# Optimization experiments

Hardware: AMD Instinct MI355X
Metric: run time of the kernel (lower is better)

## Reference

```python
import jax, jax.numpy as jnp
import numpy as np

M, N, DV, DC, ITERS = 512, 1024, 3, 6, 10
BATCH = 8192
ATANH_CLIP = 0.999995


def _build_graph():
    """Deterministic (3,6)-regular Tanner graph, edge order = row-major nonzeros of H."""
    offsets = [0, 1, 2, 512, 515, 519]
    H = np.zeros((M, N), np.int64)
    r = np.arange(M)
    for off in offsets:
        H[r, (2 * r + off) % N] = 1
    ei, ej = np.nonzero(H)                       # E = M*DC = 3072 edges, row-major
    E = ei.size
    var2edges = np.argsort(ej, kind='stable').reshape(N, DV)   # edges of each variable
    chk2edges = np.argsort(ei, kind='stable').reshape(M, DC)   # edges of each check
    v_sum = np.empty((E, DV - 1), np.int64)      # for edge e: other edges on same variable
    c_prod = np.empty((E, DC - 1), np.int64)     # for edge e: other edges on same check
    for e in range(E):
        gv = var2edges[ej[e]]
        v_sum[e] = gv[gv != e]
        gc = chk2edges[ei[e]]
        c_prod[e] = gc[gc != e]
    return v_sum, c_prod, ej.astype(np.int64), var2edges


def setup_inputs() -> dict:
    key = jax.random.key(0)
    ks = jax.random.split(key, 6)
    v_sum, c_prod, edge_var, var2edges = _build_graph()
    E = edge_var.shape[0]                        # 3072
    TW = E * (DV - 1)                            # total_weights = 6144
    return {
        "llr": jax.random.normal(ks[0], (BATCH, N), jnp.float32),
        "w_iter": 1.0 + 0.1 * jax.random.normal(ks[1], (ITERS, TW), jnp.float32),
        "llr_iter": 1.0 + 0.1 * jax.random.normal(ks[2], (ITERS, N), jnp.float32),
        "w_final": 1.0 + 0.1 * jax.random.normal(ks[3], (E,), jnp.float32),
        "llr_final": 1.0 + 0.1 * jax.random.normal(ks[4], (N,), jnp.float32),
        "v_sum_idx": jnp.asarray(v_sum),         # [E, DV-1]
        "c_prod_idx": jnp.asarray(c_prod),       # [E, DC-1]
        "edge_var": jnp.asarray(edge_var),       # [E] variable index of each edge
        "final_idx": jnp.asarray(var2edges),     # [N, DV] edges feeding each variable marginal
    }


def reference(llr, w_iter, llr_iter, w_final, llr_final,
              v_sum_idx, c_prod_idx, edge_var, final_idx):
    B = llr.shape[0]
    E = edge_var.shape[0]
    c2v0 = jnp.zeros((B, E), llr.dtype)

    def bp_iter(c2v, params):
        w, lw = params                                      # [E*(DV-1)], [N]
        # variable -> check: weighted sum of extrinsic c2v messages + weighted LLR
        s = (c2v[:, v_sum_idx] * w.reshape(E, DV - 1)).sum(-1)        # [B,E]
        v2c = jnp.tanh(0.5 * (s + (llr * lw)[:, edge_var]))           # [B,E]
        # check -> variable: product of extrinsic v2c messages, 2*atanh
        prods = v2c[:, c_prod_idx].prod(-1)                           # [B,E]
        return 2.0 * jnp.arctanh(ATANH_CLIP * prods), None

    c2v, _ = jax.lax.scan(bp_iter, c2v0, (w_iter, llr_iter))
    # final marginalization: per-variable sum of weighted incoming messages
    fin = (c2v[:, final_idx.reshape(-1)] * w_final).reshape(B, N, DV).sum(-1)
    out = fin + llr * llr_final
    return jax.nn.sigmoid(out[:, : N - M])
```

## Files before the change

### kernel.cpp

```cpp
#include <hip/hip_runtime.h>
#include <hip/hip_bf16.h>


namespace {

constexpr int T      = 512;
constexpr int ROWS   = 2;
constexpr int MCHK   = 512;
constexpr int NVAR   = 1024;
constexpr int EEDG   = 3072;
constexpr int NITER  = 10;
constexpr int STRIDE = 7;
constexpr int BATCH  = 8192;
constexpr int NOUT   = 512;

constexpr float LOG2E = 1.4426950408889634f;
constexpr float LN2   = 0.6931471805599453f;
constexpr float KAPPA = 0.999995f;

__device__ __forceinline__ float fast_exp2(float x) { return __builtin_amdgcn_exp2f(x); }
__device__ __forceinline__ float fast_log2(float x) { return __builtin_amdgcn_logf(x); }
__device__ __forceinline__ float fast_rcp (float x) { return __builtin_amdgcn_rcpf(x); }

__global__ __launch_bounds__(T, 4)
void bp_decode(const float* __restrict__ llr,
               const float* __restrict__ w_iter,
               const float* __restrict__ llr_iter,
               const float* __restrict__ w_final,
               const float* __restrict__ llr_final,
               const int*  __restrict__ v_sum_idx,
               const int*  __restrict__ edge_var,
               const int*  __restrict__ final_idx,
               float* __restrict__ out)
{
    __shared__ float2 Ad[MCHK * STRIDE];

    const int  tid = threadIdx.x;
    const long b0  = (long)blockIdx.x * ROWS;

    #pragma unroll
    for (int k = 0; k < STRIDE; ++k)
        Ad[k * T + tid] = make_float2(0.f, 0.f);

    int nb[12];
    {
        const int4* p = (const int4*)(v_sum_idx + 12 * tid);
        int4 q0 = p[0], q1 = p[1], q2 = p[2];
        nb[0]=q0.x; nb[1]=q0.y; nb[2]=q0.z; nb[3]=q0.w;
        nb[4]=q1.x; nb[5]=q1.y; nb[6]=q1.z; nb[7]=q1.w;
        nb[8]=q2.x; nb[9]=q2.y; nb[10]=q2.z; nb[11]=q2.w;
    }
    int goff[12];
    #pragma unroll
    for (int j = 0; j < 12; ++j)
        goff[j] = (nb[j] / 6) * STRIDE + (nb[j] % 6);

    int var[6];
    {
        const int2* p = (const int2*)(edge_var + 6 * tid);
        int2 q0 = p[0], q1 = p[1], q2 = p[2];
        var[0]=q0.x; var[1]=q0.y; var[2]=q1.x; var[3]=q1.y; var[4]=q2.x; var[5]=q2.y;
    }

    float Lx[6], Ly[6];
    #pragma unroll
    for (int j = 0; j < 6; ++j) {
        Lx[j] = llr[ b0      * NVAR + var[j]];
        Ly[j] = llr[(b0 + 1) * NVAR + var[j]];
    }

    __syncthreads();

    const int own = STRIDE * tid;

    #pragma unroll 1
    for (int it = 0; it < NITER; ++it) {
        const float* wit = w_iter + it * (EEDG * 2) + 12 * tid;
        float4 wa = ((const float4*)wit)[0];
        float4 wb = ((const float4*)wit)[1];
        float4 wc = ((const float4*)wit)[2];
        float w[12] = {wa.x,wa.y,wa.z,wa.w, wb.x,wb.y,wb.z,wb.w, wc.x,wc.y,wc.z,wc.w};

        const float* lit = llr_iter + it * NVAR;
        float li[6];
        #pragma unroll
        for (int j = 0; j < 6; ++j) li[j] = lit[var[j]] * LOG2E;

        float2 g[12];
        #pragma unroll
        for (int j = 0; j < 12; ++j) g[j] = Ad[goff[j]];

        __syncthreads();

        float tx[6], ty[6];
        #pragma unroll
        for (int j = 0; j < 6; ++j) {
            float ax = fmaf(w[2*j], g[2*j].x, fmaf(w[2*j+1], g[2*j+1].x, Lx[j]*li[j]));
            float ay = fmaf(w[2*j], g[2*j].y, fmaf(w[2*j+1], g[2*j+1].y, Ly[j]*li[j]));
            float zx = fast_exp2(ax);
            float zy = fast_exp2(ay);
            tx[j] = fmaf(-2.f, fast_rcp(zx + 1.f), 1.f);
            ty[j] = fmaf(-2.f, fast_rcp(zy + 1.f), 1.f);
        }

        float px[6], py[6];
        {
            float P1=tx[0], P2=P1*tx[1], P3=P2*tx[2], P4=P3*tx[3], P5=P4*tx[4];
            float S4=tx[5], S3=S4*tx[4], S2=S3*tx[3], S1=S2*tx[2], S0=S1*tx[1];
            px[0]=S0; px[1]=P1*S1; px[2]=P2*S2; px[3]=P3*S3; px[4]=P4*S4; px[5]=P5;
        }
        {
            float P1=ty[0], P2=P1*ty[1], P3=P2*ty[2], P4=P3*ty[3], P5=P4*ty[4];
            float S4=ty[5], S3=S4*ty[4], S2=S3*ty[3], S1=S2*ty[2], S0=S1*ty[1];
            py[0]=S0; py[1]=P1*S1; py[2]=P2*S2; py[3]=P3*S3; py[4]=P4*S4; py[5]=P5;
        }

        #pragma unroll
        for (int j = 0; j < 6; ++j) {
            float xx = KAPPA * px[j];
            float xy = KAPPA * py[j];
            float dx = fast_log2(1.f + xx) - fast_log2(1.f - xx);
            float dy = fast_log2(1.f + xy) - fast_log2(1.f - xy);
            Ad[own + j] = make_float2(dx, dy);
        }

        __syncthreads();
    }

    int f0 = final_idx[3*tid], f1 = final_idx[3*tid + 1], f2 = final_idx[3*tid + 2];
    float2 d0 = Ad[(f0 / 6) * STRIDE + (f0 % 6)];
    float2 d1 = Ad[(f1 / 6) * STRIDE + (f1 % 6)];
    float2 d2 = Ad[(f2 / 6) * STRIDE + (f2 % 6)];
    float wf0 = w_final[3*tid], wf1 = w_final[3*tid + 1], wf2 = w_final[3*tid + 2];
    float lf  = llr_final[tid];
    float l0  = llr[ b0      * NVAR + tid];
    float l1  = llr[(b0 + 1) * NVAR + tid];

    float finx = (d0.x*wf0 + d1.x*wf1 + d2.x*wf2) * LN2;
    float finy = (d0.y*wf0 + d1.y*wf1 + d2.y*wf2) * LN2;
    float vx = fmaf(l0, lf, finx);
    float vy = fmaf(l1, lf, finy);
    float ox = fast_rcp(1.f + fast_exp2(-vx * LOG2E));
    float oy = fast_rcp(1.f + fast_exp2(-vy * LOG2E));

    out[ b0      * NOUT + tid] = ox;
    out[(b0 + 1) * NOUT + tid] = oy;
}

}

extern "C" void kernel_launch(void* const* d_in, const int* in_sizes, int n_in,
                              void* d_out, int out_size, void* d_ws, size_t ws_size,
                              hipStream_t stream)
{
    const float* llr       = (const float*)d_in[0];
    const float* w_iter    = (const float*)d_in[1];
    const float* llr_iter  = (const float*)d_in[2];
    const float* w_final   = (const float*)d_in[3];
    const float* llr_final = (const float*)d_in[4];
    const int*   v_sum_idx = (const int*)d_in[5];
    const int*   edge_var  = (const int*)d_in[7];
    const int*   final_idx = (const int*)d_in[8];
    float* outp = (float*)d_out;

    dim3 grid(BATCH / ROWS), block(T);
    hipLaunchKernelGGL(bp_decode, grid, block, 0, stream,
                       llr, w_iter, llr_iter, w_final, llr_final,
                       v_sum_idx, edge_var, final_idx, outp);
}
```

Measured before the change: 234.8 us.

## Remove per-edge reciprocals via ratio form and pack two rows into float2 vectors

Each tanh is rewritten as (z-1)/(z+1), so the product of five tanh terms becomes a ratio of products. atanh is then computed as log2(B+κA) - log2(B-κA), which removes the reciprocal per edge. Arithmetic is moved to ext_vector float2 types so the compiler can emit packed FP32 ops (v_pk_fma/v_pk_mul) on the two batch rows. Exponentials are clamped at 2^24 to keep the products of five factors finite, which changes numerics when messages are large and could lose precision in the products.

```diff
diff --git a/kernel.cpp b/kernel.cpp
--- a/kernel.cpp
+++ b/kernel.cpp
@@ -3,6 +3,8 @@
 
 
 namespace {
+
+typedef float v2f __attribute__((ext_vector_type(2)));
 
 constexpr int T      = 512;
 constexpr int ROWS   = 2;
@@ -17,6 +19,7 @@
 constexpr float LOG2E = 1.4426950408889634f;
 constexpr float LN2   = 0.6931471805599453f;
 constexpr float KAPPA = 0.999995f;
+constexpr float ZCLMP = 16777216.0f;
 
 __device__ __forceinline__ float fast_exp2(float x) { return __builtin_amdgcn_exp2f(x); }
 __device__ __forceinline__ float fast_log2(float x) { return __builtin_amdgcn_logf(x); }
@@ -33,14 +36,14 @@
                const int*  __restrict__ final_idx,
                float* __restrict__ out)
 {
-    __shared__ float2 Ad[MCHK * STRIDE];
+    __shared__ v2f Ad[MCHK * STRIDE];
 
     const int  tid = threadIdx.x;
     const long b0  = (long)blockIdx.x * ROWS;
 
     #pragma unroll
     for (int k = 0; k < STRIDE; ++k)
-        Ad[k * T + tid] = make_float2(0.f, 0.f);
+        Ad[k * T + tid] = (v2f)(0.f);
 
     int nb[12];
     {
@@ -62,11 +65,11 @@
         var[0]=q0.x; var[1]=q0.y; var[2]=q1.x; var[3]=q1.y; var[4]=q2.x; var[5]=q2.y;
     }
 
-    float Lx[6], Ly[6];
+    v2f L[6];
     #pragma unroll
     for (int j = 0; j < 6; ++j) {
-        Lx[j] = llr[ b0      * NVAR + var[j]];
-        Ly[j] = llr[(b0 + 1) * NVAR + var[j]];
+        L[j].x = llr[ b0      * NVAR + var[j]];
+        L[j].y = llr[(b0 + 1) * NVAR + var[j]];
     }
 
     __syncthreads();
@@ -82,55 +85,58 @@
         float w[12] = {wa.x,wa.y,wa.z,wa.w, wb.x,wb.y,wb.z,wb.w, wc.x,wc.y,wc.z,wc.w};
 
         const float* lit = llr_iter + it * NVAR;
-        float li[6];
+        v2f Lli[6];
         #pragma unroll
-        for (int j = 0; j < 6; ++j) li[j] = lit[var[j]] * LOG2E;
+        for (int j = 0; j < 6; ++j) Lli[j] = L[j] * (lit[var[j]] * LOG2E);
 
-        float2 g[12];
+        v2f g[12];
         #pragma unroll
         for (int j = 0; j < 12; ++j) g[j] = Ad[goff[j]];
 
         __syncthreads();
 
-        float tx[6], ty[6];
+        v2f zm[6], zp[6];
         #pragma unroll
         for (int j = 0; j < 6; ++j) {
-            float ax = fmaf(w[2*j], g[2*j].x, fmaf(w[2*j+1], g[2*j+1].x, Lx[j]*li[j]));
-            float ay = fmaf(w[2*j], g[2*j].y, fmaf(w[2*j+1], g[2*j+1].y, Ly[j]*li[j]));
-            float zx = fast_exp2(ax);
-            float zy = fast_exp2(ay);
-            tx[j] = fmaf(-2.f, fast_rcp(zx + 1.f), 1.f);
-            ty[j] = fmaf(-2.f, fast_rcp(zy + 1.f), 1.f);
+            v2f a = w[2*j] * g[2*j] + w[2*j+1] * g[2*j+1] + Lli[j];
+            v2f z;
+            z.x = fast_exp2(a.x);
+            z.y = fast_exp2(a.y);
+            z.x = fminf(z.x, ZCLMP);
+            z.y = fminf(z.y, ZCLMP);
+            zm[j] = z - 1.f;
+            zp[j] = z + 1.f;
         }
 
-        float px[6], py[6];
+        v2f A[6], B[6];
         {
-            float P1=tx[0], P2=P1*tx[1], P3=P2*tx[2], P4=P3*tx[3], P5=P4*tx[4];
-            float S4=tx[5], S3=S4*tx[4], S2=S3*tx[3], S1=S2*tx[2], S0=S1*tx[1];
-            px[0]=S0; px[1]=P1*S1; px[2]=P2*S2; px[3]=P3*S3; px[4]=P4*S4; px[5]=P5;
+            v2f P1=zm[0], P2=P1*zm[1], P3=P2*zm[2], P4=P3*zm[3], P5=P4*zm[4];
+            v2f S4=zm[5], S3=S4*zm[4], S2=S3*zm[3], S1=S2*zm[2], S0=S1*zm[1];
+            A[0]=S0; A[1]=P1*S1; A[2]=P2*S2; A[3]=P3*S3; A[4]=P4*S4; A[5]=P5;
         }
         {
-            float P1=ty[0], P2=P1*ty[1], P3=P2*ty[2], P4=P3*ty[3], P5=P4*ty[4];
-            float S4=ty[5], S3=S4*ty[4], S2=S3*ty[3], S1=S2*ty[2], S0=S1*ty[1];
-            py[0]=S0; py[1]=P1*S1; py[2]=P2*S2; py[3]=P3*S3; py[4]=P4*S4; py[5]=P5;
+            v2f P1=zp[0], P2=P1*zp[1], P3=P2*zp[2], P4=P3*zp[3], P5=P4*zp[4];
+            v2f S4=zp[5], S3=S4*zp[4], S2=S3*zp[3], S1=S2*zp[2], S0=S1*zp[1];
+            B[0]=S0; B[1]=P1*S1; B[2]=P2*S2; B[3]=P3*S3; B[4]=P4*S4; B[5]=P5;
         }
 
         #pragma unroll
         for (int j = 0; j < 6; ++j) {
-            float xx = KAPPA * px[j];
-            float xy = KAPPA * py[j];
-            float dx = fast_log2(1.f + xx) - fast_log2(1.f - xx);
-            float dy = fast_log2(1.f + xy) - fast_log2(1.f - xy);
-            Ad[own + j] = make_float2(dx, dy);
+            v2f num = KAPPA * A[j] + B[j];
+            v2f den = B[j] - KAPPA * A[j];
+            v2f d;
+            d.x = fast_log2(num.x) - fast_log2(den.x);
+            d.y = fast_log2(num.y) - fast_log2(den.y);
+            Ad[own + j] = d;
         }
 
         __syncthreads();
     }
 
     int f0 = final_idx[3*tid], f1 = final_idx[3*tid + 1], f2 = final_idx[3*tid + 2];
-    float2 d0 = Ad[(f0 / 6) * STRIDE + (f0 % 6)];
-    float2 d1 = Ad[(f1 / 6) * STRIDE + (f1 % 6)];
-    float2 d2 = Ad[(f2 / 6) * STRIDE + (f2 % 6)];
+    v2f d0 = Ad[(f0 / 6) * STRIDE + (f0 % 6)];
+    v2f d1 = Ad[(f1 / 6) * STRIDE + (f1 % 6)];
+    v2f d2 = Ad[(f2 / 6) * STRIDE + (f2 % 6)];
     float wf0 = w_final[3*tid], wf1 = w_final[3*tid + 1], wf2 = w_final[3*tid + 2];
     float lf  = llr_final[tid];
     float l0  = llr[ b0      * NVAR + tid];
```

Result: faster. 219.0 us (-6.7%).
